# Performance work log

Hardware: AMD Instinct MI355X
Metric: run time of the kernel (lower is better)

Reference implementation:

```python
import jax, jax.numpy as jnp
import numpy as np

K = 16        # neighbors
M = 4         # repeat count
EPS = 1e-5    # BatchNorm eps (torch default)


def setup_inputs() -> dict:
    key = jax.random.key(0)
    k1, k2, k3, k4 = jax.random.split(key, 4)
    B, N, C, Fe = 8, 8192, 64, 32  # Fe = int(channels * dim_expand)
    return {
        "xyz": jax.random.normal(k1, (B, N, 3), dtype=jnp.float32),
        "feat": jax.random.normal(k2, (B, C, N), dtype=jnp.float32),
        "bn_gamma": jnp.ones((C,), jnp.float32),
        "bn_beta": jnp.zeros((C,), jnp.float32),
        "Wg": jax.random.normal(k3, (Fe, C + 3), jnp.float32) * 0.1,   # g_func weight [out, in]
        "Wh": jax.random.normal(k4, (C, M * Fe), jnp.float32) * 0.1,   # h_func weight [out, in]
    }


def reference(xyz, feat, bn_gamma, bn_beta, Wg, Wh):
    # xyz: [B, N, 3], feat: [B, C, N]
    # --- bn0: training-mode BatchNorm1d over channel dim (stats over B, N) ---
    mean = feat.mean(axis=(0, 2), keepdims=True)
    var = feat.var(axis=(0, 2), keepdims=True)
    fbn = bn_gamma[None, :, None] * (feat - mean) * jax.lax.rsqrt(var + EPS) + bn_beta[None, :, None]

    # --- g_func on concat(feat_bn, xyz^T) -> feat0 [B, N, Fe] ---
    cat = jnp.concatenate([fbn, jnp.transpose(xyz, (0, 2, 1))], axis=1)  # [B, C+3, N]
    feat0 = jnp.einsum('bcn,ec->bne', cat, Wg)                           # [B, N, Fe]

    # --- bknn: pairwise squared distances, top-k of -dist (computed once) ---
    xx = jnp.sum(xyz * xyz, axis=-1)                                     # [B, N]
    dist = xx[:, :, None] - 2.0 * jnp.einsum('bnd,bmd->bnm', xyz, xyz) + xx[:, None, :]
    _, idx = jax.lax.top_k(-dist, K)                                     # [B, N, K] int32

    # --- gather neighbor features, max-pool over K ---
    group = jax.vmap(lambda f, i: f[i])(feat0, idx)                      # [B, N, K, Fe]
    gmax = group.max(axis=2)                                             # [B, N, Fe]
    rel = gmax - feat0                                                   # [B, N, Fe]

    # Original loop reuses cached idx and feat0 every iteration, so all M
    # concatenated blocks are identical -> tile along the feature dim.
    rel_rep = jnp.concatenate([rel] * M, axis=-1)                        # [B, N, M*Fe]

    # --- h_func -> output [B, C, N] ---
    out = jnp.einsum('bnf,cf->bcn', rel_rep, Wh)
    return out
```

## Files before the change

### kernel.cpp

```cpp
#include <hip/hip_runtime.h>
#include <math.h>

#define BB 8
#define NN 8192
#define CC 64
#define FE 32
#define KN 16
#define CP3 67
#define QPW 4
#define WPB 4
#define CAPQ 64
#define YB 32
#define ZB 32
#define NCELL (YB * ZB)

__device__ float g_wsf[128];
__device__ float g_feat0[BB * NN * FE];
__device__ int   g_idx[BB * NN * KN];
__device__ float4 g_sorted[BB * NN];
__device__ int    g_sorig[BB * NN];
__device__ unsigned g_binoff[BB * (NCELL + 1)];

__device__ __forceinline__ int cbin(float v) {
    int bi = (int)((v + 4.5f) * (32.0f / 9.0f));
    if (bi < 0) bi = 0;
    if (bi > 31) bi = 31;
    return bi;
}
__device__ __forceinline__ float frz_xx(float x, float y, float z) {
    return __fmaf_rn(z, z, __fmaf_rn(y, y, __fmul_rn(x, x)));
}

__global__ __launch_bounds__(1024) void k_bnstats(const float* __restrict__ feat,
        const float* __restrict__ gamma, const float* __restrict__ beta) {
    int c = blockIdx.x;
    int tid = threadIdx.x;
    double s = 0.0, s2 = 0.0;
    for (int b = 0; b < BB; ++b) {
        const float* p = feat + ((size_t)(b * CC + c)) * NN;
        for (int n = tid; n < NN; n += 1024) {
            double v = (double)p[n];
            s += v; s2 += v * v;
        }
    }
    __shared__ double sh[1024], sh2[1024];
    sh[tid] = s; sh2[tid] = s2;
    __syncthreads();
    for (int off = 512; off > 0; off >>= 1) {
        if (tid < off) { sh[tid] += sh[tid + off]; sh2[tid] += sh2[tid + off]; }
        __syncthreads();
    }
    if (tid == 0) {
        double inv = 1.0 / (double)(BB * NN);
        double mean = sh[0] * inv;
        double var = sh2[0] * inv - mean * mean;
        float sc = gamma[c] * (float)(1.0 / sqrt(var + (double)1e-5f));
        g_wsf[c] = sc;
        g_wsf[64 + c] = beta[c] - sc * (float)mean;
    }
}

__global__ __launch_bounds__(1024) void k_zbin(const float* __restrict__ xyz) {
    __shared__ unsigned hist[NCELL];
    __shared__ unsigned scan[NCELL];
    __shared__ unsigned boff[NCELL + 1];
    int b = blockIdx.x;
    int tid = threadIdx.x;
    hist[tid] = 0;
    __syncthreads();
    const float* bx = xyz + (size_t)b * NN * 3;
    for (int n = tid; n < NN; n += 1024) {
        float y = bx[n * 3 + 1], z = bx[n * 3 + 2];
        atomicAdd(&hist[cbin(y) * ZB + cbin(z)], 1u);
    }
    __syncthreads();
    scan[tid] = hist[tid];
    __syncthreads();
    for (int off = 1; off < NCELL; off <<= 1) {
        unsigned add = (tid >= off) ? scan[tid - off] : 0u;
        __syncthreads();
        scan[tid] += add;
        __syncthreads();
    }
    if (tid == 0) boff[0] = 0;
    boff[tid + 1] = scan[tid];
    __syncthreads();
    hist[tid] = 0;
    g_binoff[b * (NCELL + 1) + tid + 1] = boff[tid + 1];
    if (tid == 0) g_binoff[b * (NCELL + 1)] = 0;
    __syncthreads();
    for (int n = tid; n < NN; n += 1024) {
        const float* p = bx + (size_t)n * 3;
        float x = p[0], y = p[1], z = p[2];
        int cell = cbin(y) * ZB + cbin(z);
        unsigned pos = boff[cell] + atomicAdd(&hist[cell], 1u);
        g_sorted[(size_t)b * NN + pos] = make_float4(x, y, z, frz_xx(x, y, z));
        g_sorig[(size_t)b * NN + pos] = n;
    }
}

__global__ __launch_bounds__(256) void k_feat0(const float* __restrict__ feat,
        const float* __restrict__ xyz, const float* __restrict__ Wg) {
    __shared__ float wgs[CP3 * FE];
    __shared__ float bias0[FE];
    int tid = threadIdx.x;
    for (int i = tid; i < CP3 * FE; i += 256) {
        int c = i >> 5, e = i & 31;
        float w = Wg[e * CP3 + c];
        if (c < CC) w *= g_wsf[c];
        wgs[c * FE + e] = w;
    }
    if (tid < FE) {
        float sacc = 0.f;
        for (int c = 0; c < CC; ++c) sacc = fmaf(Wg[tid * CP3 + c], g_wsf[64 + c], sacc);
        bias0[tid] = sacc;
    }
    __syncthreads();
    int b = blockIdx.x >> 5;
    int n = ((blockIdx.x & 31) << 8) + tid;
    const float* pz = xyz + ((size_t)(b * NN + n)) * 3;
    float x = pz[0], y = pz[1], z = pz[2];

    float acc[FE];
    #pragma unroll
    for (int e = 0; e < FE; ++e) acc[e] = bias0[e];
    const float* fp = feat + (size_t)b * CC * NN + n;
    for (int c = 0; c < CC; ++c) {
        float v = fp[(size_t)c * NN];
        const float4* w4 = (const float4*)(wgs + c * FE);
        #pragma unroll
        for (int e0 = 0; e0 < 8; ++e0) {
            float4 w = w4[e0];
            acc[e0 * 4 + 0] = fmaf(w.x, v, acc[e0 * 4 + 0]);
            acc[e0 * 4 + 1] = fmaf(w.y, v, acc[e0 * 4 + 1]);
            acc[e0 * 4 + 2] = fmaf(w.z, v, acc[e0 * 4 + 2]);
            acc[e0 * 4 + 3] = fmaf(w.w, v, acc[e0 * 4 + 3]);
        }
    }
    #pragma unroll
    for (int d = 0; d < 3; ++d) {
        float v = (d == 0) ? x : ((d == 1) ? y : z);
        const float4* w4 = (const float4*)(wgs + (CC + d) * FE);
        #pragma unroll
        for (int e0 = 0; e0 < 8; ++e0) {
            float4 w = w4[e0];
            acc[e0 * 4 + 0] = fmaf(w.x, v, acc[e0 * 4 + 0]);
            acc[e0 * 4 + 1] = fmaf(w.y, v, acc[e0 * 4 + 1]);
            acc[e0 * 4 + 2] = fmaf(w.z, v, acc[e0 * 4 + 2]);
            acc[e0 * 4 + 3] = fmaf(w.w, v, acc[e0 * 4 + 3]);
        }
    }
    float4* outp = (float4*)(g_feat0 + ((size_t)(b * NN + n)) * FE);
    #pragma unroll
    for (int e0 = 0; e0 < 8; ++e0)
        outp[e0] = make_float4(acc[e0 * 4 + 0], acc[e0 * 4 + 1], acc[e0 * 4 + 2], acc[e0 * 4 + 3]);
}

__global__ __launch_bounds__(256) void k_knn() {
    __shared__ unsigned long long qbuf[WPB * CAPQ];
    int tid = threadIdx.x;
    int lane = tid & 63;
    int w = tid >> 6;
    int wid = blockIdx.x * WPB + w;
    int b = wid >> 11;
    int g = wid & 2047;
    const float4* S = g_sorted + (size_t)b * NN;
    const int* SO = g_sorig + (size_t)b * NN;
    const unsigned* BO = g_binoff + b * (NCELL + 1);
    unsigned long long lt = (1ull << lane) - 1ull;
    unsigned long long* pb = qbuf + w * CAPQ;

    #pragma unroll 1
    for (int i = 0; i < QPW; ++i) {
        int qrank = g + (i << 11);
        float4 qv = S[qrank];
        float qx = qv.x, qy = qv.y, qz = qv.z, qxx = qv.w;
        int qorig = SO[qrank];
        float tt = 0.053f * __expf(qxx * (1.0f / 3.0f));
        float t0 = tt > 3.f ? 3.f : tt;
        float tlo = 0.f, thi = 0.f;
        unsigned cnt = 0;

        for (int attempt = 0; attempt < 40; ++attempt) {
            cnt = 0;
            float R = __fsqrt_rn(t0 + 1e-3f) + 1e-3f;
            int ylo = cbin(qy - R), yhi = cbin(qy + R);
            int zlo = cbin(qz - R), zhi = cbin(qz + R);

            for (int yb = ylo; yb <= yhi; ++yb) {
                int lo = (int)BO[yb * ZB + zlo];
                int hi = (int)BO[yb * ZB + zhi + 1];
                if (lo >= hi) continue;
                int p = lo;
                int jc = p + lane; if (jc > hi - 1) jc = hi - 1;
                float4 cur = S[jc];
                bool inc = (p + lane) < hi;
                while (p < hi) {
                    int pn = p + 64;
                    float4 nxt = cur; int jn = jc; bool inn = false;
                    if (pn < hi) {
                        jn = pn + lane; if (jn > hi - 1) jn = hi - 1;
                        nxt = S[jn];
                        inn = (pn + lane) < hi;
                    }
                    float dot = __fmaf_rn(qz, cur.z, __fmaf_rn(qy, cur.y, __fmul_rn(qx, cur.x)));
                    float dist = __fadd_rn(__fmaf_rn(-2.f, dot, qxx), cur.w);
                    bool pr = (dist <= t0) && inc;
                    unsigned long long mask = __ballot(pr);
                    if (mask) {
                        unsigned pos = cnt + (unsigned)__popcll(mask & lt);
                        if (pr && pos < CAPQ) {
                            int corig = SO[jc];
                            int db = __float_as_int(dist);
                            unsigned key = (unsigned)db ^ (unsigned)((db >> 31) | 0x80000000);
                            pb[pos] = ((unsigned long long)key << 32) | (unsigned)corig;
                        }
                        cnt += (unsigned)__popcll(mask);
                    }
                    p = pn; cur = nxt; jc = jn; inc = inn;
                }
            }
            if (cnt < KN) {
                tlo = t0;
                t0 = (thi > 0.f) ? __fsqrt_rn(tlo * thi) : t0 * 2.0f;
            } else if (cnt > CAPQ) {
                thi = t0;
                t0 = (tlo > 0.f) ? __fsqrt_rn(tlo * thi) : t0 * 0.5f;
            } else break;
        }

        unsigned tot = cnt > CAPQ ? CAPQ : cnt;
        unsigned long long e0 = ((unsigned)lane < tot) ? pb[lane] : ~0ull;
        unsigned rank0 = 0;
        for (unsigned jx = 0; jx < tot; ++jx) {
            unsigned long long v = pb[jx];
            rank0 += (v < e0) ? 1u : 0u;
        }
        if (((unsigned)lane < tot) && rank0 < KN)
            g_idx[(b * NN + qorig) * KN + rank0] = (int)(e0 & 0xffffffffull);
    }
}

__global__ __launch_bounds__(256) void k_out(const float* __restrict__ Wh,
        float* __restrict__ out) {
    __shared__ float whs[CC * FE];
    int tid = threadIdx.x;
    for (int i = tid; i < CC * FE; i += 256) {
        int c = i >> 5, e = i & 31;
        float s = 0.f;
        #pragma unroll
        for (int m = 0; m < 4; ++m) s += Wh[c * 128 + m * 32 + e];
        whs[i] = s;
    }
    __syncthreads();
    int b = blockIdx.x >> 5;
    int n = ((blockIdx.x & 31) << 8) + tid;
    const int* ip = g_idx + (size_t)(b * NN + n) * KN;
    const float4* f0 = (const float4*)(g_feat0 + (size_t)b * NN * FE);
    float gmax[FE];
    #pragma unroll
    for (int e = 0; e < FE; ++e) gmax[e] = -__builtin_inff();
    for (int k = 0; k < KN; ++k) {
        int id = ip[k] & (NN - 1);
        const float4* row = f0 + (size_t)id * 8;
        #pragma unroll
        for (int e0 = 0; e0 < 8; ++e0) {
            float4 v = row[e0];
            gmax[e0 * 4 + 0] = fmaxf(gmax[e0 * 4 + 0], v.x);
            gmax[e0 * 4 + 1] = fmaxf(gmax[e0 * 4 + 1], v.y);
            gmax[e0 * 4 + 2] = fmaxf(gmax[e0 * 4 + 2], v.z);
            gmax[e0 * 4 + 3] = fmaxf(gmax[e0 * 4 + 3], v.w);
        }
    }
    const float4* selfr = f0 + (size_t)n * 8;
    float rel[FE];
    #pragma unroll
    for (int e0 = 0; e0 < 8; ++e0) {
        float4 v = selfr[e0];
        rel[e0 * 4 + 0] = gmax[e0 * 4 + 0] - v.x;
        rel[e0 * 4 + 1] = gmax[e0 * 4 + 1] - v.y;
        rel[e0 * 4 + 2] = gmax[e0 * 4 + 2] - v.z;
        rel[e0 * 4 + 3] = gmax[e0 * 4 + 3] - v.w;
    }
    float* op = out + (size_t)b * CC * NN + n;
    for (int c = 0; c < CC; ++c) {
        const float4* w4 = (const float4*)(whs + c * FE);
        float s = 0.f;
        #pragma unroll
        for (int e0 = 0; e0 < 8; ++e0) {
            float4 w = w4[e0];
            s = fmaf(w.x, rel[e0 * 4 + 0], s);
            s = fmaf(w.y, rel[e0 * 4 + 1], s);
            s = fmaf(w.z, rel[e0 * 4 + 2], s);
            s = fmaf(w.w, rel[e0 * 4 + 3], s);
        }
        op[(size_t)c * NN] = s;
    }
}

extern "C" void kernel_launch(void* const* d_in, const int* in_sizes, int n_in,
                              void* d_out, int out_size, void* d_ws, size_t ws_size,
                              hipStream_t stream) {
    const float* xyz   = (const float*)d_in[0];
    const float* feat  = (const float*)d_in[1];
    const float* gamma = (const float*)d_in[2];
    const float* beta  = (const float*)d_in[3];
    const float* Wg    = (const float*)d_in[4];
    const float* Wh    = (const float*)d_in[5];
    float* out = (float*)d_out;
    (void)d_ws; (void)ws_size;

    hipLaunchKernelGGL(k_bnstats, dim3(64),   dim3(1024), 0, stream, feat, gamma, beta);
    hipLaunchKernelGGL(k_zbin,    dim3(8),    dim3(1024), 0, stream, xyz);
    hipLaunchKernelGGL(k_feat0,   dim3(256),  dim3(256),  0, stream, feat, xyz, Wg);
    hipLaunchKernelGGL(k_knn,     dim3(4096), dim3(256),  0, stream);
    hipLaunchKernelGGL(k_out,     dim3(256),  dim3(256),  0, stream, Wh, out);
}
```

Baseline: 209.5 us.

## Split BN stats across batch blocks and flatten KNN cell-row scan pipeline

BatchNorm statistics are now computed by 512 blocks, one per (batch, channel) pair, writing partial double sums. The feat0 kernel combines these partials and derives scale and shift itself, so the work is spread over more of the GPU instead of 64 large blocks. In the KNN search, the per-cell-row loop becomes a single flattened loop whose prefetch of the next 64 candidates can cross into the next non-empty y-row. This removes pipeline restarts and the extra loads at each row boundary, at the cost of more complex control flow.

```diff
diff --git a/kernel.cpp b/kernel.cpp
--- a/kernel.cpp
+++ b/kernel.cpp
@@ -14,7 +14,7 @@
 #define ZB 32
 #define NCELL (YB * ZB)
 
-__device__ float g_wsf[128];
+__device__ double g_part[BB * CC * 2];
 __device__ float g_feat0[BB * NN * FE];
 __device__ int   g_idx[BB * NN * KN];
 __device__ float4 g_sorted[BB * NN];
@@ -31,32 +31,25 @@
     return __fmaf_rn(z, z, __fmaf_rn(y, y, __fmul_rn(x, x)));
 }
 
-__global__ __launch_bounds__(1024) void k_bnstats(const float* __restrict__ feat,
-        const float* __restrict__ gamma, const float* __restrict__ beta) {
-    int c = blockIdx.x;
+__global__ __launch_bounds__(256) void k_bnstats(const float* __restrict__ feat) {
+    int bc = blockIdx.x;
+    const float* p = feat + (size_t)bc * NN;
     int tid = threadIdx.x;
     double s = 0.0, s2 = 0.0;
-    for (int b = 0; b < BB; ++b) {
-        const float* p = feat + ((size_t)(b * CC + c)) * NN;
-        for (int n = tid; n < NN; n += 1024) {
-            double v = (double)p[n];
-            s += v; s2 += v * v;
-        }
-    }
-    __shared__ double sh[1024], sh2[1024];
+    for (int n = tid; n < NN; n += 256) {
+        double v = (double)p[n];
+        s += v; s2 += v * v;
+    }
+    __shared__ double sh[256], sh2[256];
     sh[tid] = s; sh2[tid] = s2;
     __syncthreads();
-    for (int off = 512; off > 0; off >>= 1) {
+    for (int off = 128; off > 0; off >>= 1) {
         if (tid < off) { sh[tid] += sh[tid + off]; sh2[tid] += sh2[tid + off]; }
         __syncthreads();
     }
     if (tid == 0) {
-        double inv = 1.0 / (double)(BB * NN);
-        double mean = sh[0] * inv;
-        double var = sh2[0] * inv - mean * mean;
-        float sc = gamma[c] * (float)(1.0 / sqrt(var + (double)1e-5f));
-        g_wsf[c] = sc;
-        g_wsf[64 + c] = beta[c] - sc * (float)mean;
+        g_part[bc * 2]     = sh[0];
+        g_part[bc * 2 + 1] = sh2[0];
     }
 }
 
@@ -100,19 +93,35 @@
 }
 
 __global__ __launch_bounds__(256) void k_feat0(const float* __restrict__ feat,
-        const float* __restrict__ xyz, const float* __restrict__ Wg) {
+        const float* __restrict__ xyz, const float* __restrict__ Wg,
+        const float* __restrict__ gamma, const float* __restrict__ beta) {
+    __shared__ float scs[CC], shs[CC];
     __shared__ float wgs[CP3 * FE];
     __shared__ float bias0[FE];
     int tid = threadIdx.x;
+    if (tid < CC) {
+        double s = 0.0, s2 = 0.0;
+        for (int bb2 = 0; bb2 < BB; ++bb2) {
+            s  += g_part[((bb2 << 6) + tid) * 2];
+            s2 += g_part[((bb2 << 6) + tid) * 2 + 1];
+        }
+        double inv = 1.0 / (double)(BB * NN);
+        double mean = s * inv;
+        double var = s2 * inv - mean * mean;
+        float sc = gamma[tid] * (float)(1.0 / sqrt(var + (double)1e-5f));
+        scs[tid] = sc;
+        shs[tid] = beta[tid] - sc * (float)mean;
+    }
+    __syncthreads();
     for (int i = tid; i < CP3 * FE; i += 256) {
         int c = i >> 5, e = i & 31;
         float w = Wg[e * CP3 + c];
-        if (c < CC) w *= g_wsf[c];
+        if (c < CC) w *= scs[c];
         wgs[c * FE + e] = w;
     }
     if (tid < FE) {
         float sacc = 0.f;
-        for (int c = 0; c < CC; ++c) sacc = fmaf(Wg[tid * CP3 + c], g_wsf[64 + c], sacc);
+        for (int c = 0; c < CC; ++c) sacc = fmaf(Wg[tid * CP3 + c], shs[c], sacc);
         bias0[tid] = sacc;
     }
     __syncthreads();
@@ -187,38 +196,51 @@
             int ylo = cbin(qy - R), yhi = cbin(qy + R);
             int zlo = cbin(qz - R), zhi = cbin(qz + R);
 
-            for (int yb = ylo; yb <= yhi; ++yb) {
-                int lo = (int)BO[yb * ZB + zlo];
-                int hi = (int)BO[yb * ZB + zhi + 1];
-                if (lo >= hi) continue;
-                int p = lo;
-                int jc = p + lane; if (jc > hi - 1) jc = hi - 1;
-                float4 cur = S[jc];
-                bool inc = (p + lane) < hi;
-                while (p < hi) {
-                    int pn = p + 64;
-                    float4 nxt = cur; int jn = jc; bool inn = false;
-                    if (pn < hi) {
-                        jn = pn + lane; if (jn > hi - 1) jn = hi - 1;
-                        nxt = S[jn];
-                        inn = (pn + lane) < hi;
+            int yb = ylo;
+            int p = (int)BO[yb * ZB + zlo];
+            int hi = (int)BO[yb * ZB + zhi + 1];
+            while (p >= hi && yb < yhi) {
+                ++yb;
+                p = (int)BO[yb * ZB + zlo];
+                hi = (int)BO[yb * ZB + zhi + 1];
+            }
+            bool have = p < hi;
+            int jc = 0; float4 cur; bool inc = false;
+            if (have) {
+                jc = p + lane; if (jc > hi - 1) jc = hi - 1;
+                cur = S[jc];
+                inc = (p + lane) < hi;
+            }
+            while (have) {
+                int yb2 = yb, p2 = p + 64, hi2 = hi;
+                while (p2 >= hi2 && yb2 < yhi) {
+                    ++yb2;
+                    p2 = (int)BO[yb2 * ZB + zlo];
+                    hi2 = (int)BO[yb2 * ZB + zhi + 1];
+                }
+                bool have2 = p2 < hi2;
+                int jn = jc; float4 nxt = cur; bool inn = false;
+                if (have2) {
+                    jn = p2 + lane; if (jn > hi2 - 1) jn = hi2 - 1;
+                    nxt = S[jn];
+                    inn = (p2 + lane) < hi2;
+                }
+                float dot = __fmaf_rn(qz, cur.z, __fmaf_rn(qy, cur.y, __fmul_rn(qx, cur.x)));
+                float dist = __fadd_rn(__fmaf_rn(-2.f, dot, qxx), cur.w);
+                bool pr = (dist <= t0) && inc;
+                unsigned long long mask = __ballot(pr);
+                if (mask) {
+                    unsigned pos = cnt + (unsigned)__popcll(mask & lt);
+                    if (pr && pos < CAPQ) {
+                        int corig = SO[jc];
+                        int db = __float_as_int(dist);
+                        unsigned key = (unsigned)db ^ (unsigned)((db >> 31) | 0x80000000);
+                        pb[pos] = ((unsigned long long)key << 32) | (unsigned)corig;
                     }
-                    float dot = __fmaf_rn(qz, cur.z, __fmaf_rn(qy, cur.y, __fmul_rn(qx, cur.x)));
-                    float dist = __fadd_rn(__fmaf_rn(-2.f, dot, qxx), cur.w);
-                    bool pr = (dist <= t0) && inc;
-                    unsigned long long mask = __ballot(pr);
-                    if (mask) {
-                        unsigned pos = cnt + (unsigned)__popcll(mask & lt);
-                        if (pr && pos < CAPQ) {
-                            int corig = SO[jc];
-                            int db = __float_as_int(dist);
-                            unsigned key = (unsigned)db ^ (unsigned)((db >> 31) | 0x80000000);
-                            pb[pos] = ((unsigned long long)key << 32) | (unsigned)corig;
-                        }
-                        cnt += (unsigned)__popcll(mask);
-                    }
-                    p = pn; cur = nxt; jc = jn; inc = inn;
+                    cnt += (unsigned)__popcll(mask);
                 }
+                yb = yb2; p = p2; hi = hi2; have = have2;
+                jc = jn; cur = nxt; inc = inn;
             }
             if (cnt < KN) {
                 tlo = t0;
@@ -310,9 +332,9 @@
     float* out = (float*)d_out;
     (void)d_ws; (void)ws_size;
 
-    hipLaunchKernelGGL(k_bnstats, dim3(64),   dim3(1024), 0, stream, feat, gamma, beta);
+    hipLaunchKernelGGL(k_bnstats, dim3(512),  dim3(256),  0, stream, feat);
     hipLaunchKernelGGL(k_zbin,    dim3(8),    dim3(1024), 0, stream, xyz);
-    hipLaunchKernelGGL(k_feat0,   dim3(256),  dim3(256),  0, stream, feat, xyz, Wg);
+    hipLaunchKernelGGL(k_feat0,   dim3(256),  dim3(256),  0, stream, feat, xyz, Wg, gamma, beta);
     hipLaunchKernelGGL(k_knn,     dim3(4096), dim3(256),  0, stream);
     hipLaunchKernelGGL(k_out,     dim3(256),  dim3(256),  0, stream, Wh, out);
 }
```

New measurement: 207.3 us. No clear change (-1.0%).
